# Kernel optimization log

Measured on AMD Instinct MI355X. Metric: run time of the kernel, lower is better.

Reference implementation:

```python
import jax, jax.numpy as jnp
import numpy as np

MAX_LEVELS = 5
CHANNELS = 3


def _gauss_kernel(channels=CHANNELS):
    k = np.array([[1., 4., 6., 4., 1.],
                  [4., 16., 24., 16., 4.],
                  [6., 24., 36., 24., 6.],
                  [4., 16., 24., 16., 4.],
                  [1., 4., 6., 4., 1.]], dtype=np.float32) / 256.0
    return jnp.asarray(np.tile(k[None, None], (channels, 1, 1, 1)))  # (C,1,5,5)


def conv_gauss(img, kernel):
    # reflect-pad by 2 then depthwise 5x5 conv (groups = C)
    img = jnp.pad(img, ((0, 0), (0, 0), (2, 2), (2, 2)), mode='reflect')
    return jax.lax.conv_general_dilated(
        img, kernel, window_strides=(1, 1), padding='VALID',
        dimension_numbers=('NCHW', 'OIHW', 'NCHW'),
        feature_group_count=img.shape[1])


def downsample(x):
    return x[:, :, ::2, ::2]


def upsample(x, kernel):
    # zero-stuff: x at even (h,w) positions, zeros elsewhere, then smooth with 4*kernel
    b, c, h, w = x.shape
    up = jnp.zeros((b, c, 2 * h, 2 * w), dtype=x.dtype).at[:, :, ::2, ::2].set(x)
    return conv_gauss(up, 4.0 * kernel)


def laplacian_pyramid(img, kernel, max_levels=MAX_LEVELS):
    current = img
    pyr = []
    for _ in range(max_levels):
        filtered = conv_gauss(current, kernel)
        down = downsample(filtered)
        up = upsample(down, kernel)
        pyr.append(current - up)
        current = down
    return pyr


def setup_inputs() -> dict:
    key = jax.random.key(0)
    k1, k2 = jax.random.split(key)
    shape = (32, 3, 512, 512)
    return {
        'input': jax.random.normal(k1, shape, dtype=jnp.float32),
        'target': jax.random.normal(k2, shape, dtype=jnp.float32),
        'kernel': _gauss_kernel(CHANNELS),
    }


def reference(input, target, kernel):
    pyr_in = laplacian_pyramid(input, kernel, MAX_LEVELS)
    pyr_tg = laplacian_pyramid(target, kernel, MAX_LEVELS)
    # F.l1_loss default reduction: mean over all elements, per level
    return sum(jnp.mean(jnp.abs(a - b)) for a, b in zip(pyr_in, pyr_tg))
```

## Files before the change

### kernel.cpp

```cpp
#include <hip/hip_runtime.h>


#define BC 96
#define KA 0.0625f
#define KB 0.25f
#define KC 0.375f

__device__ __forceinline__ int refl(int i, int n) {
    if (i < 0) i = -i;
    if (i >= n) i = 2 * n - 2 - i;
    return i;
}

template<int H, int NC, bool DIFF>
__device__ __forceinline__ void load_raw(const float* __restrict__ pa,
                                         const float* __restrict__ pb,
                                         int r, int basec,
                                         float* __restrict__ a,
                                         float* __restrict__ b) {
    const int off = r * H + basec;
    if constexpr (NC == 8) {
        float4 a0 = *(const float4*)(pa + off);
        float4 a1 = *(const float4*)(pa + off + 4);
        a[0]=a0.x; a[1]=a0.y; a[2]=a0.z; a[3]=a0.w;
        a[4]=a1.x; a[5]=a1.y; a[6]=a1.z; a[7]=a1.w;
        if constexpr (DIFF) {
            float4 b0 = *(const float4*)(pb + off);
            float4 b1 = *(const float4*)(pb + off + 4);
            b[0]=b0.x; b[1]=b0.y; b[2]=b0.z; b[3]=b0.w;
            b[4]=b1.x; b[5]=b1.y; b[6]=b1.z; b[7]=b1.w;
        }
    } else if constexpr (NC == 4) {
        float4 a0 = *(const float4*)(pa + off);
        a[0]=a0.x; a[1]=a0.y; a[2]=a0.z; a[3]=a0.w;
        if constexpr (DIFF) {
            float4 b0 = *(const float4*)(pb + off);
            b[0]=b0.x; b[1]=b0.y; b[2]=b0.z; b[3]=b0.w;
        }
    } else {
        float2 a0 = *(const float2*)(pa + off);
        a[0]=a0.x; a[1]=a0.y;
        if constexpr (DIFF) {
            float2 b0 = *(const float2*)(pb + off);
            b[0]=b0.x; b[1]=b0.y;
        }
    }
}

template<int NC, bool DIFF>
__device__ __forceinline__ void materialize(const float* __restrict__ a,
                                            const float* __restrict__ b,
                                            float* __restrict__ c) {
#pragma unroll
    for (int i = 0; i < NC; ++i) c[i] = DIFF ? (a[i] - b[i]) : a[i];
}

template<int NC>
__device__ __forceinline__ void hconv(const float* __restrict__ c,
                                      float* __restrict__ o, int lane) {
    constexpr int ND = NC / 2;
    float e[NC + 3];
#pragma unroll
    for (int i = 0; i < NC; ++i) e[i + 2] = c[i];
    const bool l0 = (lane == 0), l63 = (lane == 63);
    { float v = __shfl(e[NC + 1], lane - 1); e[1] = l0 ? e[3] : v; }
    if constexpr (NC >= 4) {
        { float v = __shfl(e[NC], lane - 1); e[0] = l0 ? e[4] : v; }
        { float v = __shfl(e[2], lane + 1); e[NC + 2] = l63 ? e[NC] : v; }
    } else {
        e[0] = __shfl(e[2], l0 ? 1 : lane - 1);
        e[NC + 2] = __shfl(e[2], l63 ? 63 : lane + 1);
    }
#pragma unroll
    for (int j = 0; j < ND; ++j)
        o[j] = KA * e[2*j] + KB * e[2*j+1] + KC * e[2*j+2]
             + KB * e[2*j+3] + KA * e[2*j+4];
}

template<int H, int NC, bool DIFF, int R>
__global__ __launch_bounds__(256) void lap_slide(
        const float* __restrict__ A, const float* __restrict__ B,
        float* __restrict__ down, float* __restrict__ out, float invN) {
    constexpr int Hd = H / 2, ND = NC / 2, SPP = H / R;
    constexpr int CNT2 = R / 4 + 1;
    __shared__ float red[4];
    const int tid = threadIdx.x;
    const int lane = tid & 63, wid = tid >> 6;
    const int sid = blockIdx.x * 4 + wid;
    const int bc = sid / SPP;
    const int y0 = (sid % SPP) * R;
    const float* pa = A + (size_t)bc * H * H;
    const float* pb = DIFF ? (B + (size_t)bc * H * H) : nullptr;
    float* pd = down + (size_t)bc * Hd * Hd;
    const int basec = lane * NC;

    float h0[ND], h1[ND], h2[ND], h3[ND], h4[ND];
    float wPrev[NC], pA[NC], pB[NC], pC[NC];
    float UA1[NC], UA2[NC], VA1[NC], VA2[NC];
    float UB1[DIFF ? NC : 1], UB2[DIFF ? NC : 1];
    float VB1[DIFF ? NC : 1], VB2[DIFF ? NC : 1];
#pragma unroll
    for (int i = 0; i < NC; ++i) {
        wPrev[i] = 0.f; pA[i] = 0.f; pB[i] = 0.f; pC[i] = 0.f;
    }
    float acc = 0.f;

    const int d0 = y0 >> 1;
    const int db = d0 - 1;

    {
        float t[NC], tb[DIFF ? NC : 1], c[NC];
        load_raw<H,NC,DIFF>(pa, pb, refl(2*db - 2, H), basec, t, tb);
        materialize<NC,DIFF>(t, tb, c); hconv<NC>(c, h0, lane);
        load_raw<H,NC,DIFF>(pa, pb, refl(2*db - 1, H), basec, t, tb);
        materialize<NC,DIFF>(t, tb, c); hconv<NC>(c, h1, lane);
        load_raw<H,NC,DIFF>(pa, pb, refl(2*db, H), basec, t, tb);
        materialize<NC,DIFF>(t, tb, c); hconv<NC>(c, h2, lane);
    }
    load_raw<H,NC,DIFF>(pa, pb, refl(2*db + 1, H), basec, UA1, UB1);
    load_raw<H,NC,DIFF>(pa, pb, refl(2*db + 2, H), basec, UA2, UB2);
    load_raw<H,NC,DIFF>(pa, pb, refl(2*db + 3, H), basec, VA1, VB1);
    load_raw<H,NC,DIFF>(pa, pb, refl(2*db + 4, H), basec, VA2, VB2);

    auto body = [&](int d, float* A1, float* A2, float* B1, float* B2,
                    bool doFin, bool doStore, bool doIssue) {
        float c1[NC], c2[NC];
        materialize<NC,DIFF>(A1, B1, c1);
        materialize<NC,DIFF>(A2, B2, c2);
        if (doIssue) {
            load_raw<H,NC,DIFF>(pa, pb, refl(2*d + 5, H), basec, A1, B1);
            load_raw<H,NC,DIFF>(pa, pb, refl(2*d + 6, H), basec, A2, B2);
        }
        hconv<NC>(c1, h3, lane);
        hconv<NC>(c2, h4, lane);

        float dn[ND];
#pragma unroll
        for (int j = 0; j < ND; ++j)
            dn[j] = KA*h0[j] + KB*h1[j] + KC*h2[j] + KB*h3[j] + KA*h4[j];

        if (doStore) {
            const int doff = d * Hd + lane * ND;
            if constexpr (ND == 4) {
                float4 s; s.x=dn[0]; s.y=dn[1]; s.z=dn[2]; s.w=dn[3];
                *(float4*)(pd + doff) = s;
            } else if constexpr (ND == 2) {
                float2 s; s.x=dn[0]; s.y=dn[1];
                *(float2*)(pd + doff) = s;
            } else {
                pd[doff] = dn[0];
            }
        }

        float dm, dp;
        if constexpr (ND >= 2) {
            { float v = __shfl(dn[ND-1], lane - 1); dm = (lane == 0)  ? dn[1]    : v; }
            { float v = __shfl(dn[0],    lane + 1); dp = (lane == 63) ? dn[ND-1] : v; }
        } else {
            dm = __shfl(dn[0], (lane == 0)  ? 1  : lane - 1);
            dp = __shfl(dn[0], (lane == 63) ? 63 : lane + 1);
        }
        float wN[NC];
#pragma unroll
        for (int j = 0; j < ND; ++j) {
            float lf = j ? dn[j-1] : dm;
            float rg = (j + 1 < ND) ? dn[j+1] : dp;
            wN[2*j]     = 0.125f * lf + 0.75f * dn[j] + 0.125f * rg;
            wN[2*j + 1] = 0.5f * (dn[j] + rg);
        }

        if (doFin) {
#pragma unroll
            for (int i = 0; i < NC; ++i) {
                acc += fabsf(pA[i] - (0.75f*wPrev[i] + 0.125f*wN[i]));
                acc += fabsf(pB[i] - 0.5f*wN[i]);
            }
        }

#pragma unroll
        for (int i = 0; i < NC; ++i) {
            pA[i] = pC[i];
            pC[i] = c2[i] - 0.125f * wN[i];
            pB[i] = c1[i] - 0.5f   * wN[i];
            wPrev[i] = wN[i];
        }
#pragma unroll
        for (int j = 0; j < ND; ++j) { h0[j] = h2[j]; h1[j] = h3[j]; h2[j] = h4[j]; }
    };

#pragma unroll
    for (int i = 0; i < CNT2; ++i) {
        const bool fin = (i >= 1);
        const bool iss = (i < CNT2 - 1);
        body(db + 2*i,     UA1, UA2, UB1, UB2, fin, i >= 1,       iss);
        body(db + 2*i + 1, VA1, VA2, VB1, VB2, fin, i < CNT2 - 1, iss);
    }

#pragma unroll
    for (int off2 = 32; off2 > 0; off2 >>= 1)
        acc += __shfl_down(acc, off2, 64);
    if (lane == 0) red[wid] = acc;
    __syncthreads();
    if (tid == 0)
        atomicAdd(out, (red[0] + red[1] + red[2] + red[3]) * invN);
}

__global__ __launch_bounds__(1024) void lap_small(
        const float* __restrict__ dsrc, float* __restrict__ out,
        float invN3, float invN4) {
    __shared__ float p[64 * 66];
    __shared__ float hh[64 * 34];
    __shared__ float dd[32 * 34];
    __shared__ float W3[32 * 64];
    __shared__ float h4[32 * 18];
    __shared__ float d4[16 * 18];
    __shared__ float W4[16 * 32];
    __shared__ float red[16];
    const int tid = threadIdx.x;
    const float* src = dsrc + (size_t)blockIdx.x * 4096;
    for (int i = tid; i < 4096; i += 1024)
        p[(i >> 6) * 66 + (i & 63)] = src[i];
    __syncthreads();
    const float k[5] = {KA, KB, KC, KB, KA};
    for (int i = tid; i < 64 * 32; i += 1024) {
        int r = i >> 5, t = i & 31;
        const float* pr = p + r * 66;
        float s = 0.f;
#pragma unroll
        for (int v = 0; v < 5; ++v) s += k[v] * pr[refl(2*t + v - 2, 64)];
        hh[r * 34 + t] = s;
    }
    __syncthreads();
    for (int i = tid; i < 32 * 32; i += 1024) {
        int dy = i >> 5, t = i & 31;
        float s = 0.f;
#pragma unroll
        for (int u = 0; u < 5; ++u) s += k[u] * hh[refl(2*dy + u - 2, 64) * 34 + t];
        dd[dy * 34 + t] = s;
    }
    __syncthreads();
    for (int i = tid; i < 32 * 32; i += 1024) {
        int a = i >> 5, t = i & 31;
        const float* dr = dd + a * 34;
        float dm = dr[t == 0 ? 1 : t - 1];
        float dc = dr[t];
        float dp = dr[t == 31 ? 31 : t + 1];
        W3[a * 64 + 2*t]     = 0.125f * dm + 0.75f * dc + 0.125f * dp;
        W3[a * 64 + 2*t + 1] = 0.5f * (dc + dp);
    }
    __syncthreads();
    float acc3 = 0.f;
    for (int i = tid; i < 4096; i += 1024) {
        int y = i >> 6, x = i & 63;
        float cur = p[y * 66 + x];
        float up;
        if ((y & 1) == 0) {
            int a0 = refl(y - 2, 64) >> 1, a1 = y >> 1, a2 = refl(y + 2, 64) >> 1;
            up = 0.125f*W3[a0*64 + x] + 0.75f*W3[a1*64 + x] + 0.125f*W3[a2*64 + x];
        } else {
            int a0 = (y - 1) >> 1, a1 = refl(y + 1, 64) >> 1;
            up = 0.5f * (W3[a0*64 + x] + W3[a1*64 + x]);
        }
        acc3 += fabsf(cur - up);
    }
    __syncthreads();
    for (int i = tid; i < 32 * 16; i += 1024) {
        int r = i >> 4, t = i & 15;
        const float* pr = dd + r * 34;
        float s = 0.f;
#pragma unroll
        for (int v = 0; v < 5; ++v) s += k[v] * pr[refl(2*t + v - 2, 32)];
        h4[r * 18 + t] = s;
    }
    __syncthreads();
    for (int i = tid; i < 16 * 16; i += 1024) {
        int dy = i >> 4, t = i & 15;
        float s = 0.f;
#pragma unroll
        for (int u = 0; u < 5; ++u) s += k[u] * h4[refl(2*dy + u - 2, 32) * 18 + t];
        d4[dy * 18 + t] = s;
    }
    __syncthreads();
    for (int i = tid; i < 16 * 16; i += 1024) {
        int a = i >> 4, t = i & 15;
        const float* dr = d4 + a * 18;
        float dm = dr[t == 0 ? 1 : t - 1];
        float dc = dr[t];
        float dp = dr[t == 15 ? 15 : t + 1];
        W4[a * 32 + 2*t]     = 0.125f * dm + 0.75f * dc + 0.125f * dp;
        W4[a * 32 + 2*t + 1] = 0.5f * (dc + dp);
    }
    __syncthreads();
    float acc4 = 0.f;
    for (int i = tid; i < 1024; i += 1024) {
        int y = i >> 5, x = i & 31;
        float cur = dd[y * 34 + x];
        float up;
        if ((y & 1) == 0) {
            int a0 = refl(y - 2, 32) >> 1, a1 = y >> 1, a2 = refl(y + 2, 32) >> 1;
            up = 0.125f*W4[a0*32 + x] + 0.75f*W4[a1*32 + x] + 0.125f*W4[a2*32 + x];
        } else {
            int a0 = (y - 1) >> 1, a1 = refl(y + 1, 32) >> 1;
            up = 0.5f * (W4[a0*32 + x] + W4[a1*32 + x]);
        }
        acc4 += fabsf(cur - up);
    }
    float acc = acc3 * invN3 + acc4 * invN4;
#pragma unroll
    for (int off2 = 32; off2 > 0; off2 >>= 1)
        acc += __shfl_down(acc, off2, 64);
    int lane = tid & 63, wid = tid >> 6;
    if (lane == 0) red[wid] = acc;
    __syncthreads();
    if (tid == 0) {
        float s = 0.f;
#pragma unroll
        for (int i = 0; i < 16; ++i) s += red[i];
        atomicAdd(out, s);
    }
}

extern "C" void kernel_launch(void* const* d_in, const int* in_sizes, int n_in,
                              void* d_out, int out_size, void* d_ws, size_t ws_size,
                              hipStream_t stream) {
    const float* in = (const float*)d_in[0];
    const float* tg = (const float*)d_in[1];
    float* out = (float*)d_out;
    float* ws = (float*)d_ws;

    float* down0 = ws;
    float* down1 = down0 + (size_t)BC * 256 * 256;
    float* down2 = down1 + (size_t)BC * 128 * 128;

    hipMemsetAsync(out, 0, sizeof(float), stream);

    lap_slide<512, 8, true, 16><<<96 * 32 / 4, 256, 0, stream>>>(
        in, tg, down0, out, 1.f / (96.f * 512.f * 512.f));
    lap_slide<256, 4, false, 8><<<96 * 32 / 4, 256, 0, stream>>>(
        down0, nullptr, down1, out, 1.f / (96.f * 256.f * 256.f));
    lap_slide<128, 2, false, 4><<<96 * 32 / 4, 256, 0, stream>>>(
        down1, nullptr, down2, out, 1.f / (96.f * 128.f * 128.f));
    lap_small<<<BC, 1024, 0, stream>>>(
        down2, out, 1.f / (96.f * 64.f * 64.f), 1.f / (96.f * 32.f * 32.f));
}
```

Measured before the change: 264.3 us.

## Fuse pyramid levels 1-2 into the small-level kernel via shared memory

The sliding-window strip routine is pulled out into a reusable device function. A new per-image kernel (one 1024-thread block per batch-channel) runs levels 1 and 2 with it, keeping the level-1 downsample in a 64 KB LDS buffer and writing the level-2 result straight into the padded tile used for levels 3-4. This removes two kernel launches and the global write and re-read of the down1 and down2 intermediates. In exchange, level-1 work now runs on only 96 blocks, which may leave much of the GPU idle, and the larger LDS footprint limits occupancy.

```diff
diff --git a/kernel.cpp b/kernel.cpp
--- a/kernel.cpp
+++ b/kernel.cpp
@@ -12,13 +12,13 @@
     return i;
 }
 
-template<int H, int NC, bool DIFF>
+template<int SS, int NC, bool DIFF>
 __device__ __forceinline__ void load_raw(const float* __restrict__ pa,
                                          const float* __restrict__ pb,
                                          int r, int basec,
                                          float* __restrict__ a,
                                          float* __restrict__ b) {
-    const int off = r * H + basec;
+    const int off = r * SS + basec;
     if constexpr (NC == 8) {
         float4 a0 = *(const float4*)(pa + off);
         float4 a1 = *(const float4*)(pa + off + 4);
@@ -77,12 +77,123 @@
              + KB * e[2*j+3] + KA * e[2*j+4];
 }
 
+template<int H, int NC, int R, int SS, int DS, bool DIFF>
+__device__ __forceinline__ float slide_strip(
+        const float* __restrict__ pa, const float* __restrict__ pb,
+        float* __restrict__ pd, int lane, int y0) {
+    constexpr int ND = NC / 2;
+    constexpr int CNT2 = R / 4 + 1;
+    const int basec = lane * NC;
+
+    float h0[ND], h1[ND], h2[ND], h3[ND], h4[ND];
+    float wPrev[NC], pA[NC], pB[NC], pC[NC];
+    float UA1[NC], UA2[NC], VA1[NC], VA2[NC];
+    float UB1[DIFF ? NC : 1], UB2[DIFF ? NC : 1];
+    float VB1[DIFF ? NC : 1], VB2[DIFF ? NC : 1];
+#pragma unroll
+    for (int i = 0; i < NC; ++i) {
+        wPrev[i] = 0.f; pA[i] = 0.f; pB[i] = 0.f; pC[i] = 0.f;
+    }
+    float acc = 0.f;
+
+    const int d0 = y0 >> 1;
+    const int db = d0 - 1;
+
+    {
+        float t[NC], tb[DIFF ? NC : 1], c[NC];
+        load_raw<SS,NC,DIFF>(pa, pb, refl(2*db - 2, H), basec, t, tb);
+        materialize<NC,DIFF>(t, tb, c); hconv<NC>(c, h0, lane);
+        load_raw<SS,NC,DIFF>(pa, pb, refl(2*db - 1, H), basec, t, tb);
+        materialize<NC,DIFF>(t, tb, c); hconv<NC>(c, h1, lane);
+        load_raw<SS,NC,DIFF>(pa, pb, refl(2*db, H), basec, t, tb);
+        materialize<NC,DIFF>(t, tb, c); hconv<NC>(c, h2, lane);
+    }
+    load_raw<SS,NC,DIFF>(pa, pb, refl(2*db + 1, H), basec, UA1, UB1);
+    load_raw<SS,NC,DIFF>(pa, pb, refl(2*db + 2, H), basec, UA2, UB2);
+    load_raw<SS,NC,DIFF>(pa, pb, refl(2*db + 3, H), basec, VA1, VB1);
+    load_raw<SS,NC,DIFF>(pa, pb, refl(2*db + 4, H), basec, VA2, VB2);
+
+    auto body = [&](int d, float* A1, float* A2, float* B1, float* B2,
+                    bool doFin, bool doStore, bool doIssue) {
+        float c1[NC], c2[NC];
+        materialize<NC,DIFF>(A1, B1, c1);
+        materialize<NC,DIFF>(A2, B2, c2);
+        if (doIssue) {
+            load_raw<SS,NC,DIFF>(pa, pb, refl(2*d + 5, H), basec, A1, B1);
+            load_raw<SS,NC,DIFF>(pa, pb, refl(2*d + 6, H), basec, A2, B2);
+        }
+        hconv<NC>(c1, h3, lane);
+        hconv<NC>(c2, h4, lane);
+
+        float dn[ND];
+#pragma unroll
+        for (int j = 0; j < ND; ++j)
+            dn[j] = KA*h0[j] + KB*h1[j] + KC*h2[j] + KB*h3[j] + KA*h4[j];
+
+        if (doStore) {
+            const int doff = d * DS + lane * ND;
+            if constexpr (ND == 4) {
+                float4 s; s.x=dn[0]; s.y=dn[1]; s.z=dn[2]; s.w=dn[3];
+                *(float4*)(pd + doff) = s;
+            } else if constexpr (ND == 2) {
+                float2 s; s.x=dn[0]; s.y=dn[1];
+                *(float2*)(pd + doff) = s;
+            } else {
+                pd[doff] = dn[0];
+            }
+        }
+
+        float dm, dp;
+        if constexpr (ND >= 2) {
+            { float v = __shfl(dn[ND-1], lane - 1); dm = (lane == 0)  ? dn[1]    : v; }
+            { float v = __shfl(dn[0],    lane + 1); dp = (lane == 63) ? dn[ND-1] : v; }
+        } else {
+            dm = __shfl(dn[0], (lane == 0)  ? 1  : lane - 1);
+            dp = __shfl(dn[0], (lane == 63) ? 63 : lane + 1);
+        }
+        float wN[NC];
+#pragma unroll
+        for (int j = 0; j < ND; ++j) {
+            float lf = j ? dn[j-1] : dm;
+            float rg = (j + 1 < ND) ? dn[j+1] : dp;
+            wN[2*j]     = 0.125f * lf + 0.75f * dn[j] + 0.125f * rg;
+            wN[2*j + 1] = 0.5f * (dn[j] + rg);
+        }
+
+        if (doFin) {
+#pragma unroll
+            for (int i = 0; i < NC; ++i) {
+                acc += fabsf(pA[i] - (0.75f*wPrev[i] + 0.125f*wN[i]));
+                acc += fabsf(pB[i] - 0.5f*wN[i]);
+            }
+        }
+
+#pragma unroll
+        for (int i = 0; i < NC; ++i) {
+            pA[i] = pC[i];
+            pC[i] = c2[i] - 0.125f * wN[i];
+            pB[i] = c1[i] - 0.5f   * wN[i];
+            wPrev[i] = wN[i];
+        }
+#pragma unroll
+        for (int j = 0; j < ND; ++j) { h0[j] = h2[j]; h1[j] = h3[j]; h2[j] = h4[j]; }
+    };
+
+#pragma unroll
+    for (int i = 0; i < CNT2; ++i) {
+        const bool fin = (i >= 1);
+        const bool iss = (i < CNT2 - 1);
+        body(db + 2*i,     UA1, UA2, UB1, UB2, fin, i >= 1,       iss);
+        body(db + 2*i + 1, VA1, VA2, VB1, VB2, fin, i < CNT2 - 1, iss);
+    }
+    return acc;
+}
+
 template<int H, int NC, bool DIFF, int R>
 __global__ __launch_bounds__(256) void lap_slide(
         const float* __restrict__ A, const float* __restrict__ B,
         float* __restrict__ down, float* __restrict__ out, float invN) {
-    constexpr int Hd = H / 2, ND = NC / 2, SPP = H / R;
-    constexpr int CNT2 = R / 4 + 1;
+    constexpr int Hd = H / 2, SPP = H / R;
     __shared__ float red[4];
     const int tid = threadIdx.x;
     const int lane = tid & 63, wid = tid >> 6;
@@ -92,109 +203,8 @@
     const float* pa = A + (size_t)bc * H * H;
     const float* pb = DIFF ? (B + (size_t)bc * H * H) : nullptr;
     float* pd = down + (size_t)bc * Hd * Hd;
-    const int basec = lane * NC;
-
-    float h0[ND], h1[ND], h2[ND], h3[ND], h4[ND];
-    float wPrev[NC], pA[NC], pB[NC], pC[NC];
-    float UA1[NC], UA2[NC], VA1[NC], VA2[NC];
-    float UB1[DIFF ? NC : 1], UB2[DIFF ? NC : 1];
-    float VB1[DIFF ? NC : 1], VB2[DIFF ? NC : 1];
-#pragma unroll
-    for (int i = 0; i < NC; ++i) {
-        wPrev[i] = 0.f; pA[i] = 0.f; pB[i] = 0.f; pC[i] = 0.f;
-    }
-    float acc = 0.f;
-
-    const int d0 = y0 >> 1;
-    const int db = d0 - 1;
-
-    {
-        float t[NC], tb[DIFF ? NC : 1], c[NC];
-        load_raw<H,NC,DIFF>(pa, pb, refl(2*db - 2, H), basec, t, tb);
-        materialize<NC,DIFF>(t, tb, c); hconv<NC>(c, h0, lane);
-        load_raw<H,NC,DIFF>(pa, pb, refl(2*db - 1, H), basec, t, tb);
-        materialize<NC,DIFF>(t, tb, c); hconv<NC>(c, h1, lane);
-        load_raw<H,NC,DIFF>(pa, pb, refl(2*db, H), basec, t, tb);
-        materialize<NC,DIFF>(t, tb, c); hconv<NC>(c, h2, lane);
-    }
-    load_raw<H,NC,DIFF>(pa, pb, refl(2*db + 1, H), basec, UA1, UB1);
-    load_raw<H,NC,DIFF>(pa, pb, refl(2*db + 2, H), basec, UA2, UB2);
-    load_raw<H,NC,DIFF>(pa, pb, refl(2*db + 3, H), basec, VA1, VB1);
-    load_raw<H,NC,DIFF>(pa, pb, refl(2*db + 4, H), basec, VA2, VB2);
-
-    auto body = [&](int d, float* A1, float* A2, float* B1, float* B2,
-                    bool doFin, bool doStore, bool doIssue) {
-        float c1[NC], c2[NC];
-        materialize<NC,DIFF>(A1, B1, c1);
-        materialize<NC,DIFF>(A2, B2, c2);
-        if (doIssue) {
-            load_raw<H,NC,DIFF>(pa, pb, refl(2*d + 5, H), basec, A1, B1);
-            load_raw<H,NC,DIFF>(pa, pb, refl(2*d + 6, H), basec, A2, B2);
-        }
-        hconv<NC>(c1, h3, lane);
-        hconv<NC>(c2, h4, lane);
-
-        float dn[ND];
-#pragma unroll
-        for (int j = 0; j < ND; ++j)
-            dn[j] = KA*h0[j] + KB*h1[j] + KC*h2[j] + KB*h3[j] + KA*h4[j];
-
-        if (doStore) {
-            const int doff = d * Hd + lane * ND;
-            if constexpr (ND == 4) {
-                float4 s; s.x=dn[0]; s.y=dn[1]; s.z=dn[2]; s.w=dn[3];
-                *(float4*)(pd + doff) = s;
-            } else if constexpr (ND == 2) {
-                float2 s; s.x=dn[0]; s.y=dn[1];
-                *(float2*)(pd + doff) = s;
-            } else {
-                pd[doff] = dn[0];
-            }
-        }
-
-        float dm, dp;
-        if constexpr (ND >= 2) {
-            { float v = __shfl(dn[ND-1], lane - 1); dm = (lane == 0)  ? dn[1]    : v; }
-            { float v = __shfl(dn[0],    lane + 1); dp = (lane == 63) ? dn[ND-1] : v; }
-        } else {
-            dm = __shfl(dn[0], (lane == 0)  ? 1  : lane - 1);
-            dp = __shfl(dn[0], (lane == 63) ? 63 : lane + 1);
-        }
-        float wN[NC];
-#pragma unroll
-        for (int j = 0; j < ND; ++j) {
-            float lf = j ? dn[j-1] : dm;
-            float rg = (j + 1 < ND) ? dn[j+1] : dp;
-            wN[2*j]     = 0.125f * lf + 0.75f * dn[j] + 0.125f * rg;
-            wN[2*j + 1] = 0.5f * (dn[j] + rg);
-        }
-
-        if (doFin) {
-#pragma unroll
-            for (int i = 0; i < NC; ++i) {
-                acc += fabsf(pA[i] - (0.75f*wPrev[i] + 0.125f*wN[i]));
-                acc += fabsf(pB[i] - 0.5f*wN[i]);
-            }
-        }
-
-#pragma unroll
-        for (int i = 0; i < NC; ++i) {
-            pA[i] = pC[i];
-            pC[i] = c2[i] - 0.125f * wN[i];
-            pB[i] = c1[i] - 0.5f   * wN[i];
-            wPrev[i] = wN[i];
-        }
-#pragma unroll
-        for (int j = 0; j < ND; ++j) { h0[j] = h2[j]; h1[j] = h3[j]; h2[j] = h4[j]; }
-    };
-
-#pragma unroll
-    for (int i = 0; i < CNT2; ++i) {
-        const bool fin = (i >= 1);
-        const bool iss = (i < CNT2 - 1);
-        body(db + 2*i,     UA1, UA2, UB1, UB2, fin, i >= 1,       iss);
-        body(db + 2*i + 1, VA1, VA2, VB1, VB2, fin, i < CNT2 - 1, iss);
-    }
+
+    float acc = slide_strip<H, NC, R, H, Hd, DIFF>(pa, pb, pd, lane, y0);
 
 #pragma unroll
     for (int off2 = 32; off2 > 0; off2 >>= 1)
@@ -205,9 +215,10 @@
         atomicAdd(out, (red[0] + red[1] + red[2] + red[3]) * invN);
 }
 
-__global__ __launch_bounds__(1024) void lap_small(
-        const float* __restrict__ dsrc, float* __restrict__ out,
-        float invN3, float invN4) {
+__global__ __launch_bounds__(1024) void lap_rest(
+        const float* __restrict__ down0, float* __restrict__ out,
+        float invN1, float invN2, float invN3, float invN4) {
+    __shared__ float d1[128 * 128];
     __shared__ float p[64 * 66];
     __shared__ float hh[64 * 34];
     __shared__ float dd[32 * 34];
@@ -217,10 +228,16 @@
     __shared__ float W4[16 * 32];
     __shared__ float red[16];
     const int tid = threadIdx.x;
-    const float* src = dsrc + (size_t)blockIdx.x * 4096;
-    for (int i = tid; i < 4096; i += 1024)
-        p[(i >> 6) * 66 + (i & 63)] = src[i];
-    __syncthreads();
+    const int lane = tid & 63, wid = tid >> 6;
+    const float* src = down0 + (size_t)blockIdx.x * 65536;
+
+    float acc = invN1 *
+        slide_strip<256, 4, 16, 256, 128, false>(src, nullptr, d1, lane, wid * 16);
+    __syncthreads();
+    acc += invN2 *
+        slide_strip<128, 2, 8, 128, 66, false>(d1, nullptr, p, lane, wid * 8);
+    __syncthreads();
+
     const float k[5] = {KA, KB, KC, KB, KA};
     for (int i = tid; i < 64 * 32; i += 1024) {
         int r = i >> 5, t = i & 31;
@@ -305,11 +322,11 @@
         }
         acc4 += fabsf(cur - up);
     }
-    float acc = acc3 * invN3 + acc4 * invN4;
+    acc += acc3 * invN3 + acc4 * invN4;
+
 #pragma unroll
     for (int off2 = 32; off2 > 0; off2 >>= 1)
         acc += __shfl_down(acc, off2, 64);
-    int lane = tid & 63, wid = tid >> 6;
     if (lane == 0) red[wid] = acc;
     __syncthreads();
     if (tid == 0) {
@@ -329,17 +346,13 @@
     float* ws = (float*)d_ws;
 
     float* down0 = ws;
-    float* down1 = down0 + (size_t)BC * 256 * 256;
-    float* down2 = down1 + (size_t)BC * 128 * 128;
 
     hipMemsetAsync(out, 0, sizeof(float), stream);
 
     lap_slide<512, 8, true, 16><<<96 * 32 / 4, 256, 0, stream>>>(
         in, tg, down0, out, 1.f / (96.f * 512.f * 512.f));
-    lap_slide<256, 4, false, 8><<<96 * 32 / 4, 256, 0, stream>>>(
-        down0, nullptr, down1, out, 1.f / (96.f * 256.f * 256.f));
-    lap_slide<128, 2, false, 4><<<96 * 32 / 4, 256, 0, stream>>>(
-        down1, nullptr, down2, out, 1.f / (96.f * 128.f * 128.f));
-    lap_small<<<BC, 1024, 0, stream>>>(
-        down2, out, 1.f / (96.f * 64.f * 64.f), 1.f / (96.f * 32.f * 32.f));
-}
+    lap_rest<<<BC, 1024, 0, stream>>>(
+        down0, out,
+        1.f / (96.f * 256.f * 256.f), 1.f / (96.f * 128.f * 128.f),
+        1.f / (96.f * 64.f * 64.f),  1.f / (96.f * 32.f * 32.f));
+}
```

New measurement: 244.1 us. 7.7% less time.
